# Performance work log

Hardware: AMD Instinct MI355X
Metric: run time of the kernel (lower is better)

The kernel has to match this reference:

```python
import jax, jax.numpy as jnp
import numpy as np

B, FIN, FOUT, FH2, NMIX, LAT, H, W = 16, 256, 256, 256, 8, 512, 64, 64


def _xavier(key, shape):
    # xavier_normal_ over last-two-ish dims; simple fan-based scale
    fan_in = int(np.prod(shape[1:]))
    fan_out = shape[0]
    s = (2.0 / (fan_in + fan_out)) ** 0.5
    return jax.random.normal(key, shape, jnp.float32) * s


def setup_inputs() -> dict:
    key = jax.random.key(0)
    ks = jax.random.split(key, 12)
    return {
        "x": jax.random.normal(ks[0], (B, FIN, H, W), jnp.float32),
        "lat": jax.random.normal(ks[1], (B, LAT), jnp.float32),
        # mixture kernel banks [n_mix, out_ch, in_ch] (kernel_size=1 squeezed)
        "k_in_mix": _xavier(ks[2], (NMIX, FH2, FIN)),
        "k_mid_mix": _xavier(ks[3], (NMIX, FH2, 2 * FH2)),
        "k_out_mix": _xavier(ks[4], (NMIX, FOUT, 2 * FH2)),
        "k_short_mix": _xavier(ks[5], (NMIX, FOUT, FIN)),
        # mixture bias banks [n_mix, ch]
        "b_in_mix": _xavier(ks[6], (NMIX, FH2)),
        "b_mid_mix": _xavier(ks[7], (NMIX, FH2)),
        "b_out_mix": _xavier(ks[8], (NMIX, FOUT)),
        "b_short_mix": _xavier(ks[9], (NMIX, FOUT)),
        # dyna_mix = nn.Linear(lat_size, n_mix) (lat_factor=0 path)
        "w_dyna": _xavier(ks[10], (NMIX, LAT)),
        "b_dyna": jnp.zeros((NMIX,), jnp.float32),
    }


def _complex_wave(h):
    # doubles channel dim: concat(sin, cos) along channels (per sample)
    return jnp.concatenate([jnp.sin(h), jnp.cos(h)], axis=1)


def reference(x, lat, k_in_mix, k_mid_mix, k_out_mix, k_short_mix,
              b_in_mix, b_mid_mix, b_out_mix, b_short_mix, w_dyna, b_dyna):
    # mixing coefficients per sample: [B, n_mix]
    mix = lat @ w_dyna.T + b_dyna
    # per-sample 1x1 conv kernels via mixture reduction: [B, out, in]
    k_in = jnp.einsum('bm,moi->boi', mix, k_in_mix)
    k_mid = jnp.einsum('bm,moi->boi', mix, k_mid_mix)
    k_out = jnp.einsum('bm,moi->boi', mix, k_out_mix)
    k_short = jnp.einsum('bm,moi->boi', mix, k_short_mix)
    # per-sample biases: [B, ch, 1, 1]
    b_in = (mix @ b_in_mix)[:, :, None, None]
    b_mid = (mix @ b_mid_mix)[:, :, None, None]
    b_out = (mix @ b_out_mix)[:, :, None, None]
    b_short = (mix @ b_short_mix)[:, :, None, None]
    # grouped conv with groups = batch (kernel_size=1) == per-sample matmul
    short = jnp.einsum('boi,bihw->bohw', k_short, x) + b_short
    h = jnp.einsum('boi,bihw->bohw', k_in, x) + b_in            # [B, FH2, H, W]
    h = _complex_wave(h)                                        # [B, 2*FH2, H, W]
    h = jnp.einsum('boi,bihw->bohw', k_mid, h) + b_mid
    h = _complex_wave(h)
    out = jnp.einsum('boi,bihw->bohw', k_out, h) + b_out + short
    return out
```

## Files before the change

### kernel.cpp

```cpp
#include <hip/hip_runtime.h>
#include <stdint.h>

#define B_    16
#define FIN   256
#define FOUT  256
#define FH2   256
#define NMIX  8
#define LAT   512
#define HW    4096
#define MT    64

typedef short bf16x8 __attribute__((ext_vector_type(8)));
typedef float f32x4  __attribute__((ext_vector_type(4)));

#define WS_MIX    0
#define WS_BIAS   1024
#define WS_WIN    131072
#define WS_WMID   2228224
#define WS_WOUT   6422528
#define WS_WSHORT 10616832

__device__ __forceinline__ uint16_t f2bf(float f) {
  uint32_t u = __builtin_bit_cast(uint32_t, f);
  u += 0x7fffu + ((u >> 16) & 1u);
  return (uint16_t)(u >> 16);
}
__device__ __forceinline__ uint32_t pack2(float lo, float hi) {
  return (uint32_t)f2bf(lo) | ((uint32_t)f2bf(hi) << 16);
}

#define MFMA(a, b, c) __builtin_amdgcn_mfma_f32_16x16x32_bf16(a, b, c, 0, 0, 0)

__global__ void k_mix_bias(const float* __restrict__ lat,
                           const float* __restrict__ w_dyna,
                           const float* __restrict__ b_dyna,
                           const float* __restrict__ b_in_mix,
                           const float* __restrict__ b_mid_mix,
                           const float* __restrict__ b_out_mix,
                           const float* __restrict__ b_short_mix,
                           float* __restrict__ ws_mix,
                           float* __restrict__ ws_bias) {
  __shared__ float smix[NMIX];
  const int t = threadIdx.x;
  const int lane = t & 63, wv = t >> 6;
  const int b = blockIdx.x;
#pragma unroll
  for (int d2 = 0; d2 < 2; d2++) {
    int m = wv * 2 + d2;
    float s = 0.f;
#pragma unroll
    for (int j = 0; j < 8; j++)
      s += lat[b * LAT + j * 64 + lane] * w_dyna[m * LAT + j * 64 + lane];
#pragma unroll
    for (int off = 32; off; off >>= 1) s += __shfl_xor(s, off);
    if (lane == 0) {
      float v = s + b_dyna[m];
      ws_mix[b * NMIX + m] = v;
      smix[m] = v;
    }
  }
  __syncthreads();
  const float* banks[4] = {b_in_mix, b_mid_mix, b_out_mix, b_short_mix};
  for (int pos = t; pos < 1024; pos += 256) {
    int bank = pos >> 8, ch = pos & 255;
    const float* bp = banks[bank];
    float a = 0.f;
#pragma unroll
    for (int m = 0; m < NMIX; m++) a += smix[m] * bp[m * 256 + ch];
    ws_bias[(bank * B_ + b) * 256 + ch] = a;
  }
}

__global__ void k_weights(const float* __restrict__ k_in_mix,
                          const float* __restrict__ k_mid_mix,
                          const float* __restrict__ k_out_mix,
                          const float* __restrict__ k_short_mix,
                          const float* __restrict__ ws_mix,
                          uint16_t* __restrict__ w_in,
                          uint16_t* __restrict__ w_mid,
                          uint16_t* __restrict__ w_out,
                          uint16_t* __restrict__ w_short) {
  __shared__ float smix[B_ * NMIX];
  const int t = threadIdx.x;
  if (t < B_ * NMIX) smix[t] = ws_mix[t];
  __syncthreads();
  const int e8 = (blockIdx.x * 256 + t) * 8;
  const float* srcA;
  uint16_t* dst;
  int sstride, dstride;
  bool ileave;
  if (e8 < 65536) {
    int e = e8;
    int lane = (e >> 3) & 63, ots = (e >> 9) & 3, kt = (e >> 11) & 7, wv = e >> 14;
    int row = wv * 64 + ots * 16 + (lane & 15);
    int k0 = kt * 32 + (lane >> 4) * 8;
    srcA = k_in_mix + row * 256 + k0; sstride = 65536; ileave = false;
    dst = w_in + e;                   dstride = 65536;
  } else if (e8 < 196608) {
    int e = e8 - 65536;
    int lane = (e >> 3) & 63, ots = (e >> 9) & 3, kt = (e >> 11) & 15, wv = e >> 15;
    int row = wv * 64 + ots * 16 + (lane & 15);
    int kp0 = kt * 32 + (lane >> 4) * 8;
    srcA = k_mid_mix + row * 512 + (kp0 >> 1); sstride = 131072; ileave = true;
    dst = w_mid + e;                           dstride = 131072;
  } else if (e8 < 327680) {
    int e = e8 - 196608;
    int lane = (e >> 3) & 63, ots = (e >> 9) & 3, kt = (e >> 11) & 15, wv = e >> 15;
    int row = wv * 64 + ots * 16 + (lane & 15);
    int kp0 = kt * 32 + (lane >> 4) * 8;
    srcA = k_out_mix + row * 512 + (kp0 >> 1); sstride = 131072; ileave = true;
    dst = w_out + e;                           dstride = 131072;
  } else {
    int e = e8 - 327680;
    int lane = (e >> 3) & 63, ots = (e >> 9) & 3, kt = (e >> 11) & 7, wv = e >> 14;
    int row = wv * 64 + ots * 16 + (lane & 15);
    int k0 = kt * 32 + (lane >> 4) * 8;
    srcA = k_short_mix + row * 256 + k0; sstride = 65536; ileave = false;
    dst = w_short + e;                   dstride = 65536;
  }
  const int boff = ileave ? 256 : 4;
  float4 va[NMIX], vb[NMIX];
#pragma unroll
  for (int m = 0; m < NMIX; m++) {
    va[m] = *(const float4*)(srcA + m * sstride);
    vb[m] = *(const float4*)(srcA + m * sstride + boff);
  }
  for (int b = 0; b < B_; b++) {
    float4 ra = make_float4(0.f, 0.f, 0.f, 0.f), rb = ra;
#pragma unroll
    for (int m = 0; m < NMIX; m++) {
      const float s = smix[b * NMIX + m];
      ra.x += s * va[m].x; ra.y += s * va[m].y; ra.z += s * va[m].z; ra.w += s * va[m].w;
      rb.x += s * vb[m].x; rb.y += s * vb[m].y; rb.z += s * vb[m].z; rb.w += s * vb[m].w;
    }
    int4 pkt;
    if (ileave) {
      pkt = make_int4((int)pack2(ra.x, rb.x), (int)pack2(ra.y, rb.y),
                      (int)pack2(ra.z, rb.z), (int)pack2(ra.w, rb.w));
    } else {
      pkt = make_int4((int)pack2(ra.x, ra.y), (int)pack2(ra.z, ra.w),
                      (int)pack2(rb.x, rb.y), (int)pack2(rb.z, rb.w));
    }
    *(int4*)(dst + (size_t)b * dstride) = pkt;
  }
}

__launch_bounds__(256, 2)
__global__ void k_main(const float* __restrict__ x,
                       const float* __restrict__ ws_bias,
                       const uint16_t* __restrict__ w_in,
                       const uint16_t* __restrict__ w_mid,
                       const uint16_t* __restrict__ w_out,
                       const uint16_t* __restrict__ w_short,
                       float* __restrict__ out) {
  __shared__ int4 smem4[65536 / 16];
  char* lds = (char*)smem4;
  char* Xs = lds;
  char* H1 = lds;

  const int t = threadIdx.x;
  const int lane = t & 63;
  const int wv = t >> 6;
  const int q = lane >> 4;
  const int n = lane & 15;
  const int b = blockIdx.x & 15;
  const int p0 = (blockIdx.x >> 4) * MT;

  const float* xb = x + (size_t)b * FIN * HW + p0;
  const int xpos = t & 63;

  {
    float xr[8][8];
#pragma unroll
    for (int u = 0; u < 8; u++) {
      const int cg = wv * 8 + u;
#pragma unroll
      for (int e = 0; e < 8; e++)
        xr[u][e] = xb[(size_t)(cg * 8 + e) * HW + xpos];
    }
#pragma unroll
    for (int u = 0; u < 8; u++) {
      const int cg = wv * 8 + u;
      *(int4*)(Xs + xpos * 512 + ((cg ^ (xpos & 7)) * 16)) = make_int4(
          (int)pack2(xr[u][0], xr[u][1]), (int)pack2(xr[u][2], xr[u][3]),
          (int)pack2(xr[u][4], xr[u][5]), (int)pack2(xr[u][6], xr[u][7]));
    }
  }

  f32x4 acc_h[4][4], acc_s[4][4];
#pragma unroll
  for (int ots = 0; ots < 4; ots++) {
    const int o = wv * 64 + ots * 16 + q * 4;
    const float4 vi = *(const float4*)&ws_bias[(0 * B_ + b) * 256 + o];
    const float4 vs = *(const float4*)&ws_bias[(3 * B_ + b) * 256 + o];
    f32x4 ah, asv;
    ah[0] = vi.x; ah[1] = vi.y; ah[2] = vi.z; ah[3] = vi.w;
    asv[0] = vs.x; asv[1] = vs.y; asv[2] = vs.z; asv[3] = vs.w;
#pragma unroll
    for (int pt = 0; pt < 4; pt++) { acc_h[ots][pt] = ah; acc_s[ots][pt] = asv; }
  }

  const uint16_t* Wi = w_in + (size_t)b * 65536 + wv * 16384 + lane * 8;
  const uint16_t* Ws = w_short + (size_t)b * 65536 + wv * 16384 + lane * 8;
  bf16x8 ai[2][4], asf[2][4];
#pragma unroll
  for (int ots = 0; ots < 4; ots++) {
    ai[0][ots] = *(const bf16x8*)(Wi + ots * 512);
    asf[0][ots] = *(const bf16x8*)(Ws + ots * 512);
  }
  __syncthreads();

#pragma unroll
  for (int kt = 0; kt < 8; kt++) {
    if (kt < 7) {
#pragma unroll
      for (int ots = 0; ots < 4; ots++) {
        ai[(kt + 1) & 1][ots] = *(const bf16x8*)(Wi + (kt + 1) * 2048 + ots * 512);
        asf[(kt + 1) & 1][ots] = *(const bf16x8*)(Ws + (kt + 1) * 2048 + ots * 512);
      }
    }
    bf16x8 bf[4];
#pragma unroll
    for (int pt = 0; pt < 4; pt++) {
      const int p = pt * 16 + n;
      bf[pt] = *(const bf16x8*)(Xs + p * 512 + (((kt * 4 + q) ^ (p & 7)) * 16));
    }
    __builtin_amdgcn_s_setprio(1);
#pragma unroll
    for (int ots = 0; ots < 4; ots++) {
#pragma unroll
      for (int pt = 0; pt < 4; pt++) {
        acc_h[ots][pt] = MFMA(ai[kt & 1][ots], bf[pt], acc_h[ots][pt]);
        acc_s[ots][pt] = MFMA(asf[kt & 1][ots], bf[pt], acc_s[ots][pt]);
      }
    }
    __builtin_amdgcn_s_setprio(0);
  }
  __syncthreads();

#pragma unroll
  for (int ots = 0; ots < 4; ots++) {
    const int ctile = (wv * 4 + ots) * 4 + q;
#pragma unroll
    for (int pt = 0; pt < 4; pt++) {
      const int p = pt * 16 + n;
      *(int4*)(H1 + p * 1024 + ((ctile ^ (p & 7)) * 16)) = make_int4(
          (int)pack2(__sinf(acc_h[ots][pt][0]), __cosf(acc_h[ots][pt][0])),
          (int)pack2(__sinf(acc_h[ots][pt][1]), __cosf(acc_h[ots][pt][1])),
          (int)pack2(__sinf(acc_h[ots][pt][2]), __cosf(acc_h[ots][pt][2])),
          (int)pack2(__sinf(acc_h[ots][pt][3]), __cosf(acc_h[ots][pt][3])));
    }
  }

  const uint16_t* Wm = w_mid + (size_t)b * 131072 + wv * 32768 + lane * 8;
  bf16x8 am[2][4];
#pragma unroll
  for (int ots = 0; ots < 4; ots++) {
    am[0][ots] = *(const bf16x8*)(Wm + 0 * 2048 + ots * 512);
    am[1][ots] = *(const bf16x8*)(Wm + 1 * 2048 + ots * 512);
  }
  f32x4 acc2[4][4];
#pragma unroll
  for (int ots = 0; ots < 4; ots++) {
    const int o = wv * 64 + ots * 16 + q * 4;
    const float4 v = *(const float4*)&ws_bias[(1 * B_ + b) * 256 + o];
    f32x4 a2;
    a2[0] = v.x; a2[1] = v.y; a2[2] = v.z; a2[3] = v.w;
#pragma unroll
    for (int pt = 0; pt < 4; pt++) acc2[ots][pt] = a2;
  }
  __syncthreads();

  {
    bf16x8 bfP[2][4];
#pragma unroll
    for (int pt = 0; pt < 4; pt++) {
      const int p = pt * 16 + n;
      bfP[0][pt] = *(const bf16x8*)(H1 + p * 1024 + ((q ^ (p & 7)) * 16));
    }
#pragma unroll
    for (int kt = 0; kt < 16; kt++) {
      if (kt < 15) {
#pragma unroll
        for (int pt = 0; pt < 4; pt++) {
          const int p = pt * 16 + n;
          bfP[(kt + 1) & 1][pt] =
              *(const bf16x8*)(H1 + p * 1024 + ((((kt + 1) * 4 + q) ^ (p & 7)) * 16));
        }
      }
      __builtin_amdgcn_s_setprio(1);
#pragma unroll
      for (int ots = 0; ots < 4; ots++)
#pragma unroll
        for (int pt = 0; pt < 4; pt++)
          acc2[ots][pt] = MFMA(am[kt & 1][ots], bfP[kt & 1][pt], acc2[ots][pt]);
      __builtin_amdgcn_s_setprio(0);
      if (kt < 14) {
#pragma unroll
        for (int ots = 0; ots < 4; ots++)
          am[kt & 1][ots] = *(const bf16x8*)(Wm + (kt + 2) * 2048 + ots * 512);
      }
    }
  }
  __syncthreads();

#pragma unroll
  for (int ots = 0; ots < 4; ots++) {
    const int ctile = (wv * 4 + ots) * 4 + q;
#pragma unroll
    for (int pt = 0; pt < 4; pt++) {
      const int p = pt * 16 + n;
      *(int4*)(H1 + p * 1024 + ((ctile ^ (p & 7)) * 16)) = make_int4(
          (int)pack2(__sinf(acc2[ots][pt][0]), __cosf(acc2[ots][pt][0])),
          (int)pack2(__sinf(acc2[ots][pt][1]), __cosf(acc2[ots][pt][1])),
          (int)pack2(__sinf(acc2[ots][pt][2]), __cosf(acc2[ots][pt][2])),
          (int)pack2(__sinf(acc2[ots][pt][3]), __cosf(acc2[ots][pt][3])));
    }
  }

  const uint16_t* Wo = w_out + (size_t)b * 131072 + wv * 32768 + lane * 8;
  bf16x8 ao[2][4];
#pragma unroll
  for (int ots = 0; ots < 4; ots++) {
    ao[0][ots] = *(const bf16x8*)(Wo + 0 * 2048 + ots * 512);
    ao[1][ots] = *(const bf16x8*)(Wo + 1 * 2048 + ots * 512);
  }
#pragma unroll
  for (int ots = 0; ots < 4; ots++) {
    const int o = wv * 64 + ots * 16 + q * 4;
    const float4 v = *(const float4*)&ws_bias[(2 * B_ + b) * 256 + o];
#pragma unroll
    for (int pt = 0; pt < 4; pt++) {
      acc_s[ots][pt][0] += v.x; acc_s[ots][pt][1] += v.y;
      acc_s[ots][pt][2] += v.z; acc_s[ots][pt][3] += v.w;
    }
  }
  __syncthreads();

  {
    bf16x8 bfP[2][4];
#pragma unroll
    for (int pt = 0; pt < 4; pt++) {
      const int p = pt * 16 + n;
      bfP[0][pt] = *(const bf16x8*)(H1 + p * 1024 + ((q ^ (p & 7)) * 16));
    }
#pragma unroll
    for (int kt = 0; kt < 16; kt++) {
      if (kt < 15) {
#pragma unroll
        for (int pt = 0; pt < 4; pt++) {
          const int p = pt * 16 + n;
          bfP[(kt + 1) & 1][pt] =
              *(const bf16x8*)(H1 + p * 1024 + ((((kt + 1) * 4 + q) ^ (p & 7)) * 16));
        }
      }
      __builtin_amdgcn_s_setprio(1);
#pragma unroll
      for (int ots = 0; ots < 4; ots++)
#pragma unroll
        for (int pt = 0; pt < 4; pt++)
          acc_s[ots][pt] = MFMA(ao[kt & 1][ots], bfP[kt & 1][pt], acc_s[ots][pt]);
      __builtin_amdgcn_s_setprio(0);
      if (kt < 14) {
#pragma unroll
        for (int ots = 0; ots < 4; ots++)
          ao[kt & 1][ots] = *(const bf16x8*)(Wo + (kt + 2) * 2048 + ots * 512);
      }
    }
  }

  {
    float* ob = out + (size_t)b * FOUT * HW + p0;
#pragma unroll
    for (int ots = 0; ots < 4; ots++) {
#pragma unroll
      for (int pt = 0; pt < 4; pt++) {
#pragma unroll
        for (int r = 0; r < 4; r++) {
          const int o = wv * 64 + ots * 16 + q * 4 + r;
          ob[(size_t)o * HW + pt * 16 + n] = acc_s[ots][pt][r];
        }
      }
    }
  }
}

extern "C" void kernel_launch(void* const* d_in, const int* in_sizes, int n_in,
                              void* d_out, int out_size, void* d_ws, size_t ws_size,
                              hipStream_t stream) {
  const float* x           = (const float*)d_in[0];
  const float* lat         = (const float*)d_in[1];
  const float* k_in_mix    = (const float*)d_in[2];
  const float* k_mid_mix   = (const float*)d_in[3];
  const float* k_out_mix   = (const float*)d_in[4];
  const float* k_short_mix = (const float*)d_in[5];
  const float* b_in_mix    = (const float*)d_in[6];
  const float* b_mid_mix   = (const float*)d_in[7];
  const float* b_out_mix   = (const float*)d_in[8];
  const float* b_short_mix = (const float*)d_in[9];
  const float* w_dyna      = (const float*)d_in[10];
  const float* b_dyna      = (const float*)d_in[11];

  char* ws = (char*)d_ws;
  float*    ws_mix  = (float*)(ws + WS_MIX);
  float*    ws_bias = (float*)(ws + WS_BIAS);
  uint16_t* w_in    = (uint16_t*)(ws + WS_WIN);
  uint16_t* w_mid   = (uint16_t*)(ws + WS_WMID);
  uint16_t* w_out   = (uint16_t*)(ws + WS_WOUT);
  uint16_t* w_short = (uint16_t*)(ws + WS_WSHORT);
  float* out = (float*)d_out;

  hipLaunchKernelGGL(k_mix_bias, dim3(16), dim3(256), 0, stream,
                     lat, w_dyna, b_dyna, b_in_mix, b_mid_mix, b_out_mix,
                     b_short_mix, ws_mix, ws_bias);
  hipLaunchKernelGGL(k_weights, dim3(192), dim3(256), 0, stream,
                     k_in_mix, k_mid_mix, k_out_mix, k_short_mix, ws_mix,
                     w_in, w_mid, w_out, w_short);
  hipLaunchKernelGGL(k_main, dim3(1024), dim3(256), 0, stream,
                     x, ws_bias, w_in, w_mid, w_out, w_short, out);
}
```

Baseline: 190.3 us.

## Switch main kernel to 32x32x16 bf16 MFMA tiles with re-laid-out weights

Result: slower. 196.0 us (+3.0%).

```diff
diff --git a/kernel.cpp b/kernel.cpp
--- a/kernel.cpp
+++ b/kernel.cpp
@@ -12,6 +12,7 @@
 
 typedef short bf16x8 __attribute__((ext_vector_type(8)));
 typedef float f32x4  __attribute__((ext_vector_type(4)));
+typedef float f32x16 __attribute__((ext_vector_type(16)));
 
 #define WS_MIX    0
 #define WS_BIAS   1024
@@ -29,7 +30,7 @@
   return (uint32_t)f2bf(lo) | ((uint32_t)f2bf(hi) << 16);
 }
 
-#define MFMA(a, b, c) __builtin_amdgcn_mfma_f32_16x16x32_bf16(a, b, c, 0, 0, 0)
+#define MFMA32(a, b, c) __builtin_amdgcn_mfma_f32_32x32x16_bf16(a, b, c, 0, 0, 0)
 
 __global__ void k_mix_bias(const float* __restrict__ lat,
                            const float* __restrict__ w_dyna,
@@ -91,30 +92,30 @@
   bool ileave;
   if (e8 < 65536) {
     int e = e8;
-    int lane = (e >> 3) & 63, ots = (e >> 9) & 3, kt = (e >> 11) & 7, wv = e >> 14;
-    int row = wv * 64 + ots * 16 + (lane & 15);
-    int k0 = kt * 32 + (lane >> 4) * 8;
+    int lane = (e >> 3) & 63, orr = (e >> 9) & 1, kt = (e >> 10) & 15, wv = e >> 14;
+    int row = wv * 64 + orr * 32 + (lane & 31);
+    int k0 = kt * 16 + (lane >> 5) * 8;
     srcA = k_in_mix + row * 256 + k0; sstride = 65536; ileave = false;
     dst = w_in + e;                   dstride = 65536;
   } else if (e8 < 196608) {
     int e = e8 - 65536;
-    int lane = (e >> 3) & 63, ots = (e >> 9) & 3, kt = (e >> 11) & 15, wv = e >> 15;
-    int row = wv * 64 + ots * 16 + (lane & 15);
-    int kp0 = kt * 32 + (lane >> 4) * 8;
+    int lane = (e >> 3) & 63, orr = (e >> 9) & 1, kt = (e >> 10) & 31, wv = e >> 15;
+    int row = wv * 64 + orr * 32 + (lane & 31);
+    int kp0 = kt * 16 + (lane >> 5) * 8;
     srcA = k_mid_mix + row * 512 + (kp0 >> 1); sstride = 131072; ileave = true;
     dst = w_mid + e;                           dstride = 131072;
   } else if (e8 < 327680) {
     int e = e8 - 196608;
-    int lane = (e >> 3) & 63, ots = (e >> 9) & 3, kt = (e >> 11) & 15, wv = e >> 15;
-    int row = wv * 64 + ots * 16 + (lane & 15);
-    int kp0 = kt * 32 + (lane >> 4) * 8;
+    int lane = (e >> 3) & 63, orr = (e >> 9) & 1, kt = (e >> 10) & 31, wv = e >> 15;
+    int row = wv * 64 + orr * 32 + (lane & 31);
+    int kp0 = kt * 16 + (lane >> 5) * 8;
     srcA = k_out_mix + row * 512 + (kp0 >> 1); sstride = 131072; ileave = true;
     dst = w_out + e;                           dstride = 131072;
   } else {
     int e = e8 - 327680;
-    int lane = (e >> 3) & 63, ots = (e >> 9) & 3, kt = (e >> 11) & 7, wv = e >> 14;
-    int row = wv * 64 + ots * 16 + (lane & 15);
-    int k0 = kt * 32 + (lane >> 4) * 8;
+    int lane = (e >> 3) & 63, orr = (e >> 9) & 1, kt = (e >> 10) & 15, wv = e >> 14;
+    int row = wv * 64 + orr * 32 + (lane & 31);
+    int k0 = kt * 16 + (lane >> 5) * 8;
     srcA = k_short_mix + row * 256 + k0; sstride = 65536; ileave = false;
     dst = w_short + e;                   dstride = 65536;
   }
@@ -161,8 +162,8 @@
   const int t = threadIdx.x;
   const int lane = t & 63;
   const int wv = t >> 6;
-  const int q = lane >> 4;
-  const int n = lane & 15;
+  const int l31 = lane & 31;
+  const int ks = lane >> 5;
   const int b = blockIdx.x & 15;
   const int p0 = (blockIdx.x >> 4) * MT;
 
@@ -187,184 +188,221 @@
     }
   }
 
-  f32x4 acc_h[4][4], acc_s[4][4];
-#pragma unroll
-  for (int ots = 0; ots < 4; ots++) {
-    const int o = wv * 64 + ots * 16 + q * 4;
-    const float4 vi = *(const float4*)&ws_bias[(0 * B_ + b) * 256 + o];
-    const float4 vs = *(const float4*)&ws_bias[(3 * B_ + b) * 256 + o];
-    f32x4 ah, asv;
-    ah[0] = vi.x; ah[1] = vi.y; ah[2] = vi.z; ah[3] = vi.w;
-    asv[0] = vs.x; asv[1] = vs.y; asv[2] = vs.z; asv[3] = vs.w;
-#pragma unroll
-    for (int pt = 0; pt < 4; pt++) { acc_h[ots][pt] = ah; acc_s[ots][pt] = asv; }
+  f32x16 acc_h[2][2], acc_s[2][2];
+#pragma unroll
+  for (int orr = 0; orr < 2; orr++) {
+    float4 bh[4], bs[4];
+#pragma unroll
+    for (int g = 0; g < 4; g++) {
+      const int o0 = wv * 64 + orr * 32 + g * 8 + 4 * ks;
+      bh[g] = *(const float4*)&ws_bias[(0 * B_ + b) * 256 + o0];
+      bs[g] = *(const float4*)&ws_bias[(3 * B_ + b) * 256 + o0];
+    }
+#pragma unroll
+    for (int pc = 0; pc < 2; pc++) {
+#pragma unroll
+      for (int g = 0; g < 4; g++) {
+        acc_h[orr][pc][4 * g + 0] = bh[g].x; acc_h[orr][pc][4 * g + 1] = bh[g].y;
+        acc_h[orr][pc][4 * g + 2] = bh[g].z; acc_h[orr][pc][4 * g + 3] = bh[g].w;
+        acc_s[orr][pc][4 * g + 0] = bs[g].x; acc_s[orr][pc][4 * g + 1] = bs[g].y;
+        acc_s[orr][pc][4 * g + 2] = bs[g].z; acc_s[orr][pc][4 * g + 3] = bs[g].w;
+      }
+    }
   }
 
   const uint16_t* Wi = w_in + (size_t)b * 65536 + wv * 16384 + lane * 8;
   const uint16_t* Ws = w_short + (size_t)b * 65536 + wv * 16384 + lane * 8;
-  bf16x8 ai[2][4], asf[2][4];
-#pragma unroll
-  for (int ots = 0; ots < 4; ots++) {
-    ai[0][ots] = *(const bf16x8*)(Wi + ots * 512);
-    asf[0][ots] = *(const bf16x8*)(Ws + ots * 512);
-  }
-  __syncthreads();
-
-#pragma unroll
-  for (int kt = 0; kt < 8; kt++) {
-    if (kt < 7) {
-#pragma unroll
-      for (int ots = 0; ots < 4; ots++) {
-        ai[(kt + 1) & 1][ots] = *(const bf16x8*)(Wi + (kt + 1) * 2048 + ots * 512);
-        asf[(kt + 1) & 1][ots] = *(const bf16x8*)(Ws + (kt + 1) * 2048 + ots * 512);
-      }
-    }
-    bf16x8 bf[4];
-#pragma unroll
-    for (int pt = 0; pt < 4; pt++) {
-      const int p = pt * 16 + n;
-      bf[pt] = *(const bf16x8*)(Xs + p * 512 + (((kt * 4 + q) ^ (p & 7)) * 16));
+  bf16x8 ai[2][2], asf[2][2];
+#pragma unroll
+  for (int orr = 0; orr < 2; orr++) {
+    ai[0][orr] = *(const bf16x8*)(Wi + 0 * 1024 + orr * 512);
+    asf[0][orr] = *(const bf16x8*)(Ws + 0 * 1024 + orr * 512);
+    ai[1][orr] = *(const bf16x8*)(Wi + 1 * 1024 + orr * 512);
+    asf[1][orr] = *(const bf16x8*)(Ws + 1 * 1024 + orr * 512);
+  }
+  __syncthreads();
+
+#pragma unroll
+  for (int kt = 0; kt < 16; kt++) {
+    bf16x8 bf[2];
+#pragma unroll
+    for (int pc = 0; pc < 2; pc++) {
+      const int pos = pc * 32 + l31;
+      const int cg = kt * 2 + ks;
+      bf[pc] = *(const bf16x8*)(Xs + pos * 512 + ((cg ^ (pos & 7)) * 16));
     }
     __builtin_amdgcn_s_setprio(1);
 #pragma unroll
-    for (int ots = 0; ots < 4; ots++) {
-#pragma unroll
-      for (int pt = 0; pt < 4; pt++) {
-        acc_h[ots][pt] = MFMA(ai[kt & 1][ots], bf[pt], acc_h[ots][pt]);
-        acc_s[ots][pt] = MFMA(asf[kt & 1][ots], bf[pt], acc_s[ots][pt]);
+    for (int orr = 0; orr < 2; orr++) {
+#pragma unroll
+      for (int pc = 0; pc < 2; pc++) {
+        acc_h[orr][pc] = MFMA32(ai[kt & 1][orr], bf[pc], acc_h[orr][pc]);
+        acc_s[orr][pc] = MFMA32(asf[kt & 1][orr], bf[pc], acc_s[orr][pc]);
       }
     }
     __builtin_amdgcn_s_setprio(0);
-  }
-  __syncthreads();
-
-#pragma unroll
-  for (int ots = 0; ots < 4; ots++) {
-    const int ctile = (wv * 4 + ots) * 4 + q;
-#pragma unroll
-    for (int pt = 0; pt < 4; pt++) {
-      const int p = pt * 16 + n;
-      *(int4*)(H1 + p * 1024 + ((ctile ^ (p & 7)) * 16)) = make_int4(
-          (int)pack2(__sinf(acc_h[ots][pt][0]), __cosf(acc_h[ots][pt][0])),
-          (int)pack2(__sinf(acc_h[ots][pt][1]), __cosf(acc_h[ots][pt][1])),
-          (int)pack2(__sinf(acc_h[ots][pt][2]), __cosf(acc_h[ots][pt][2])),
-          (int)pack2(__sinf(acc_h[ots][pt][3]), __cosf(acc_h[ots][pt][3])));
+    if (kt < 14) {
+#pragma unroll
+      for (int orr = 0; orr < 2; orr++) {
+        ai[kt & 1][orr] = *(const bf16x8*)(Wi + (kt + 2) * 1024 + orr * 512);
+        asf[kt & 1][orr] = *(const bf16x8*)(Ws + (kt + 2) * 1024 + orr * 512);
+      }
+    }
+  }
+  __syncthreads();
+
+#pragma unroll
+  for (int orr = 0; orr < 2; orr++) {
+#pragma unroll
+    for (int pc = 0; pc < 2; pc++) {
+      const int pos = pc * 32 + l31;
+#pragma unroll
+      for (int g = 0; g < 4; g++) {
+        const int ct = wv * 16 + orr * 8 + g * 2 + ks;
+        *(int4*)(H1 + pos * 1024 + ((ct ^ (pos & 7)) * 16)) = make_int4(
+            (int)pack2(__sinf(acc_h[orr][pc][4 * g + 0]), __cosf(acc_h[orr][pc][4 * g + 0])),
+            (int)pack2(__sinf(acc_h[orr][pc][4 * g + 1]), __cosf(acc_h[orr][pc][4 * g + 1])),
+            (int)pack2(__sinf(acc_h[orr][pc][4 * g + 2]), __cosf(acc_h[orr][pc][4 * g + 2])),
+            (int)pack2(__sinf(acc_h[orr][pc][4 * g + 3]), __cosf(acc_h[orr][pc][4 * g + 3])));
+      }
     }
   }
 
   const uint16_t* Wm = w_mid + (size_t)b * 131072 + wv * 32768 + lane * 8;
-  bf16x8 am[2][4];
-#pragma unroll
-  for (int ots = 0; ots < 4; ots++) {
-    am[0][ots] = *(const bf16x8*)(Wm + 0 * 2048 + ots * 512);
-    am[1][ots] = *(const bf16x8*)(Wm + 1 * 2048 + ots * 512);
-  }
-  f32x4 acc2[4][4];
-#pragma unroll
-  for (int ots = 0; ots < 4; ots++) {
-    const int o = wv * 64 + ots * 16 + q * 4;
-    const float4 v = *(const float4*)&ws_bias[(1 * B_ + b) * 256 + o];
-    f32x4 a2;
-    a2[0] = v.x; a2[1] = v.y; a2[2] = v.z; a2[3] = v.w;
-#pragma unroll
-    for (int pt = 0; pt < 4; pt++) acc2[ots][pt] = a2;
+  bf16x8 am[3][2];
+#pragma unroll
+  for (int orr = 0; orr < 2; orr++) {
+    am[0][orr] = *(const bf16x8*)(Wm + 0 * 1024 + orr * 512);
+    am[1][orr] = *(const bf16x8*)(Wm + 1 * 1024 + orr * 512);
+    am[2][orr] = *(const bf16x8*)(Wm + 2 * 1024 + orr * 512);
+  }
+  f32x16 acc2[2][2];
+#pragma unroll
+  for (int orr = 0; orr < 2; orr++) {
+    float4 bm[4];
+#pragma unroll
+    for (int g = 0; g < 4; g++) {
+      const int o0 = wv * 64 + orr * 32 + g * 8 + 4 * ks;
+      bm[g] = *(const float4*)&ws_bias[(1 * B_ + b) * 256 + o0];
+    }
+#pragma unroll
+    for (int pc = 0; pc < 2; pc++) {
+#pragma unroll
+      for (int g = 0; g < 4; g++) {
+        acc2[orr][pc][4 * g + 0] = bm[g].x; acc2[orr][pc][4 * g + 1] = bm[g].y;
+        acc2[orr][pc][4 * g + 2] = bm[g].z; acc2[orr][pc][4 * g + 3] = bm[g].w;
+      }
+    }
   }
   __syncthreads();
 
   {
-    bf16x8 bfP[2][4];
-#pragma unroll
-    for (int pt = 0; pt < 4; pt++) {
-      const int p = pt * 16 + n;
-      bfP[0][pt] = *(const bf16x8*)(H1 + p * 1024 + ((q ^ (p & 7)) * 16));
-    }
-#pragma unroll
-    for (int kt = 0; kt < 16; kt++) {
-      if (kt < 15) {
-#pragma unroll
-        for (int pt = 0; pt < 4; pt++) {
-          const int p = pt * 16 + n;
-          bfP[(kt + 1) & 1][pt] =
-              *(const bf16x8*)(H1 + p * 1024 + ((((kt + 1) * 4 + q) ^ (p & 7)) * 16));
+    bf16x8 bfP[2][2];
+#pragma unroll
+    for (int pc = 0; pc < 2; pc++) {
+      const int pos = pc * 32 + l31;
+      bfP[0][pc] = *(const bf16x8*)(H1 + pos * 1024 + ((ks ^ (pos & 7)) * 16));
+    }
+#pragma unroll
+    for (int kt = 0; kt < 32; kt++) {
+      if (kt < 31) {
+#pragma unroll
+        for (int pc = 0; pc < 2; pc++) {
+          const int pos = pc * 32 + l31;
+          const int cg = (kt + 1) * 2 + ks;
+          bfP[(kt + 1) & 1][pc] =
+              *(const bf16x8*)(H1 + pos * 1024 + ((cg ^ (pos & 7)) * 16));
         }
       }
       __builtin_amdgcn_s_setprio(1);
 #pragma unroll
-      for (int ots = 0; ots < 4; ots++)
-#pragma unroll
-        for (int pt = 0; pt < 4; pt++)
-          acc2[ots][pt] = MFMA(am[kt & 1][ots], bfP[kt & 1][pt], acc2[ots][pt]);
+      for (int orr = 0; orr < 2; orr++)
+#pragma unroll
+        for (int pc = 0; pc < 2; pc++)
+          acc2[orr][pc] = MFMA32(am[kt % 3][orr], bfP[kt & 1][pc], acc2[orr][pc]);
       __builtin_amdgcn_s_setprio(0);
-      if (kt < 14) {
-#pragma unroll
-        for (int ots = 0; ots < 4; ots++)
-          am[kt & 1][ots] = *(const bf16x8*)(Wm + (kt + 2) * 2048 + ots * 512);
-      }
-    }
-  }
-  __syncthreads();
-
-#pragma unroll
-  for (int ots = 0; ots < 4; ots++) {
-    const int ctile = (wv * 4 + ots) * 4 + q;
-#pragma unroll
-    for (int pt = 0; pt < 4; pt++) {
-      const int p = pt * 16 + n;
-      *(int4*)(H1 + p * 1024 + ((ctile ^ (p & 7)) * 16)) = make_int4(
-          (int)pack2(__sinf(acc2[ots][pt][0]), __cosf(acc2[ots][pt][0])),
-          (int)pack2(__sinf(acc2[ots][pt][1]), __cosf(acc2[ots][pt][1])),
-          (int)pack2(__sinf(acc2[ots][pt][2]), __cosf(acc2[ots][pt][2])),
-          (int)pack2(__sinf(acc2[ots][pt][3]), __cosf(acc2[ots][pt][3])));
+      if (kt < 29) {
+#pragma unroll
+        for (int orr = 0; orr < 2; orr++)
+          am[kt % 3][orr] = *(const bf16x8*)(Wm + (kt + 3) * 1024 + orr * 512);
+      }
+    }
+  }
+  __syncthreads();
+
+#pragma unroll
+  for (int orr = 0; orr < 2; orr++) {
+#pragma unroll
+    for (int pc = 0; pc < 2; pc++) {
+      const int pos = pc * 32 + l31;
+#pragma unroll
+      for (int g = 0; g < 4; g++) {
+        const int ct = wv * 16 + orr * 8 + g * 2 + ks;
+        *(int4*)(H1 + pos * 1024 + ((ct ^ (pos & 7)) * 16)) = make_int4(
+            (int)pack2(__sinf(acc2[orr][pc][4 * g + 0]), __cosf(acc2[orr][pc][4 * g + 0])),
+            (int)pack2(__sinf(acc2[orr][pc][4 * g + 1]), __cosf(acc2[orr][pc][4 * g + 1])),
+            (int)pack2(__sinf(acc2[orr][pc][4 * g + 2]), __cosf(acc2[orr][pc][4 * g + 2])),
+            (int)pack2(__sinf(acc2[orr][pc][4 * g + 3]), __cosf(acc2[orr][pc][4 * g + 3])));
+      }
     }
   }
 
   const uint16_t* Wo = w_out + (size_t)b * 131072 + wv * 32768 + lane * 8;
-  bf16x8 ao[2][4];
-#pragma unroll
-  for (int ots = 0; ots < 4; ots++) {
-    ao[0][ots] = *(const bf16x8*)(Wo + 0 * 2048 + ots * 512);
-    ao[1][ots] = *(const bf16x8*)(Wo + 1 * 2048 + ots * 512);
-  }
-#pragma unroll
-  for (int ots = 0; ots < 4; ots++) {
-    const int o = wv * 64 + ots * 16 + q * 4;
-    const float4 v = *(const float4*)&ws_bias[(2 * B_ + b) * 256 + o];
-#pragma unroll
-    for (int pt = 0; pt < 4; pt++) {
-      acc_s[ots][pt][0] += v.x; acc_s[ots][pt][1] += v.y;
-      acc_s[ots][pt][2] += v.z; acc_s[ots][pt][3] += v.w;
+  bf16x8 ao[3][2];
+#pragma unroll
+  for (int orr = 0; orr < 2; orr++) {
+    ao[0][orr] = *(const bf16x8*)(Wo + 0 * 1024 + orr * 512);
+    ao[1][orr] = *(const bf16x8*)(Wo + 1 * 1024 + orr * 512);
+    ao[2][orr] = *(const bf16x8*)(Wo + 2 * 1024 + orr * 512);
+  }
+#pragma unroll
+  for (int orr = 0; orr < 2; orr++) {
+    float4 bo[4];
+#pragma unroll
+    for (int g = 0; g < 4; g++) {
+      const int o0 = wv * 64 + orr * 32 + g * 8 + 4 * ks;
+      bo[g] = *(const float4*)&ws_bias[(2 * B_ + b) * 256 + o0];
+    }
+#pragma unroll
+    for (int pc = 0; pc < 2; pc++) {
+#pragma unroll
+      for (int g = 0; g < 4; g++) {
+        acc_s[orr][pc][4 * g + 0] += bo[g].x; acc_s[orr][pc][4 * g + 1] += bo[g].y;
+        acc_s[orr][pc][4 * g + 2] += bo[g].z; acc_s[orr][pc][4 * g + 3] += bo[g].w;
+      }
     }
   }
   __syncthreads();
 
   {
-    bf16x8 bfP[2][4];
-#pragma unroll
-    for (int pt = 0; pt < 4; pt++) {
-      const int p = pt * 16 + n;
-      bfP[0][pt] = *(const bf16x8*)(H1 + p * 1024 + ((q ^ (p & 7)) * 16));
-    }
-#pragma unroll
-    for (int kt = 0; kt < 16; kt++) {
-      if (kt < 15) {
-#pragma unroll
-        for (int pt = 0; pt < 4; pt++) {
-          const int p = pt * 16 + n;
-          bfP[(kt + 1) & 1][pt] =
-              *(const bf16x8*)(H1 + p * 1024 + ((((kt + 1) * 4 + q) ^ (p & 7)) * 16));
+    bf16x8 bfP[2][2];
+#pragma unroll
+    for (int pc = 0; pc < 2; pc++) {
+      const int pos = pc * 32 + l31;
+      bfP[0][pc] = *(const bf16x8*)(H1 + pos * 1024 + ((ks ^ (pos & 7)) * 16));
+    }
+#pragma unroll
+    for (int kt = 0; kt < 32; kt++) {
+      if (kt < 31) {
+#pragma unroll
+        for (int pc = 0; pc < 2; pc++) {
+          const int pos = pc * 32 + l31;
+          const int cg = (kt + 1) * 2 + ks;
+          bfP[(kt + 1) & 1][pc] =
+              *(const bf16x8*)(H1 + pos * 1024 + ((cg ^ (pos & 7)) * 16));
         }
       }
       __builtin_amdgcn_s_setprio(1);
 #pragma unroll
-      for (int ots = 0; ots < 4; ots++)
-#pragma unroll
-        for (int pt = 0; pt < 4; pt++)
-          acc_s[ots][pt] = MFMA(ao[kt & 1][ots], bfP[kt & 1][pt], acc_s[ots][pt]);
+      for (int orr = 0; orr < 2; orr++)
+#pragma unroll
+        for (int pc = 0; pc < 2; pc++)
+          acc_s[orr][pc] = MFMA32(ao[kt % 3][orr], bfP[kt & 1][pc], acc_s[orr][pc]);
       __builtin_amdgcn_s_setprio(0);
-      if (kt < 14) {
-#pragma unroll
-        for (int ots = 0; ots < 4; ots++)
-          ao[kt & 1][ots] = *(const bf16x8*)(Wo + (kt + 2) * 2048 + ots * 512);
+      if (kt < 29) {
+#pragma unroll
+        for (int orr = 0; orr < 2; orr++)
+          ao[kt % 3][orr] = *(const bf16x8*)(Wo + (kt + 3) * 1024 + orr * 512);
       }
     }
   }
@@ -372,13 +410,17 @@
   {
     float* ob = out + (size_t)b * FOUT * HW + p0;
 #pragma unroll
-    for (int ots = 0; ots < 4; ots++) {
-#pragma unroll
-      for (int pt = 0; pt < 4; pt++) {
-#pragma unroll
-        for (int r = 0; r < 4; r++) {
-          const int o = wv * 64 + ots * 16 + q * 4 + r;
-          ob[(size_t)o * HW + pt * 16 + n] = acc_s[ots][pt][r];
+    for (int orr = 0; orr < 2; orr++) {
+#pragma unroll
+      for (int pc = 0; pc < 2; pc++) {
+        const int pos = pc * 32 + l31;
+#pragma unroll
+        for (int g = 0; g < 4; g++) {
+#pragma unroll
+          for (int i = 0; i < 4; i++) {
+            const int och = wv * 64 + orr * 32 + g * 8 + 4 * ks + i;
+            ob[(size_t)och * HW + pos] = acc_s[orr][pc][4 * g + i];
+          }
         }
       }
     }
```
